# Kernel tuning notes

Measured on AMD Instinct MI355X. Metric: run time of the kernel, lower is better.

Reference implementation:

```python
import jax, jax.numpy as jnp
import numpy as np

LEAKY_SLOPE = 0.01  # torch F.leaky_relu default

N_NODES = 100000
N_EDGES = 1600000
IN_CH, HID_CH, OUT_CH = 128, 64, 32


def glorot(key, shape):
    fan_in, fan_out = shape
    lim = jnp.sqrt(6.0 / (fan_in + fan_out))
    return jax.random.uniform(key, shape, jnp.float32, -lim, lim)


def setup_inputs() -> dict:
    key = jax.random.key(0)
    ks = jax.random.split(key, 10)
    x = jax.random.normal(ks[0], (N_NODES, IN_CH), jnp.float32)
    edge_index = jax.random.randint(ks[1], (2, N_EDGES), 0, N_NODES, jnp.int64)
    return {
        "x": x,
        "edge_index": edge_index,
        "W1": glorot(ks[2], (IN_CH, HID_CH)),
        "b1": jnp.zeros((HID_CH,), jnp.float32),
        "W2": glorot(ks[3], (HID_CH, HID_CH)),
        "b2": jnp.zeros((HID_CH,), jnp.float32),
        "W_mu": glorot(ks[4], (HID_CH, OUT_CH)),
        "b_mu": jnp.zeros((OUT_CH,), jnp.float32),
        "W_ls": glorot(ks[5], (HID_CH, OUT_CH)),
        "b_ls": jnp.zeros((OUT_CH,), jnp.float32),
    }


def _gcn_norm(edge_index, n_nodes):
    """Symmetric GCN normalization with self-loops (PyG GCNConv default)."""
    src, dst = edge_index[0], edge_index[1]
    ones = jnp.ones((src.shape[0],), jnp.float32)
    deg = jax.ops.segment_sum(ones, dst, num_segments=n_nodes) + 1.0  # +1 self-loop
    dis = jax.lax.rsqrt(deg)  # deg >= 1 so no div-by-zero
    edge_w = dis[src] * dis[dst]          # [E] normalization per edge
    self_w = dis * dis                    # [N] self-loop normalization
    return src, dst, edge_w, self_w


def _gcn_conv(h, W, b, src, dst, edge_w, self_w, n_nodes):
    h = h @ W                                           # [N, C_out]
    msg = h[src] * edge_w[:, None]                      # gather + scale, [E, C_out]
    agg = jax.ops.segment_sum(msg, dst, num_segments=n_nodes)
    agg = agg + h * self_w[:, None]                     # self-loop term
    return agg + b


def reference(x, edge_index, W1, b1, W2, b2, W_mu, b_mu, W_ls, b_ls):
    n = x.shape[0]
    src, dst, ew, sw = _gcn_norm(edge_index, n)
    # dropout is identity in eval mode (reference baseline)
    h = jax.nn.leaky_relu(_gcn_conv(x, W1, b1, src, dst, ew, sw, n), LEAKY_SLOPE)
    h = jax.nn.leaky_relu(_gcn_conv(h, W2, b2, src, dst, ew, sw, n), LEAKY_SLOPE)
    mu = _gcn_conv(h, W_mu, b_mu, src, dst, ew, sw, n)
    logstd = _gcn_conv(h, W_ls, b_ls, src, dst, ew, sw, n)
    return mu, logstd
```

## Files before the change

kernel.cpp:

```cpp
#include <hip/hip_runtime.h>

#define LEAKY_SLOPE 0.01f
#define CBSH 7
#define CBSZ 128
#define CHUNK 4096

__device__ __forceinline__ unsigned short f2bf(float f) {
    unsigned int u = __builtin_bit_cast(unsigned int, f);
    u = (u + 0x7FFFu + ((u >> 16) & 1u)) >> 16;
    return (unsigned short)u;
}
__device__ __forceinline__ float bf2f(unsigned short h) {
    return __builtin_bit_cast(float, ((unsigned int)h) << 16);
}
__device__ __forceinline__ float ulof(unsigned u) {
    return __builtin_bit_cast(float, u << 16);
}
__device__ __forceinline__ float uhif(unsigned u) {
    return __builtin_bit_cast(float, u & 0xFFFF0000u);
}
__device__ __forceinline__ float bcastf(int hb, int k) {
    return __builtin_bit_cast(float, __builtin_amdgcn_readlane(hb, k));
}

__global__ __launch_bounds__(256) void chist_kernel(const int* __restrict__ dst,
                                                    int* __restrict__ cbin, int E, int ncb) {
    __shared__ int bins[1024];
    for (int i = threadIdx.x; i < 1024; i += 256) bins[i] = 0;
    __syncthreads();
    int stride = gridDim.x * blockDim.x;
    for (int e = blockIdx.x * blockDim.x + threadIdx.x; e < E; e += stride)
        atomicAdd(&bins[dst[e] >> CBSH], 1);
    __syncthreads();
    for (int i = threadIdx.x; i < ncb; i += 256) {
        int v = bins[i];
        if (v) atomicAdd(&cbin[i], v);
    }
}

__global__ __launch_bounds__(256) void cscan_kernel(const int* __restrict__ cbin,
                                                    int* __restrict__ cboff,
                                                    int* __restrict__ ccur16, int ncb) {
    __shared__ int s[256];
    __shared__ int carry;
    int t = threadIdx.x;
    if (t == 0) carry = 0;
    __syncthreads();
    for (int base = 0; base < ncb; base += 256) {
        int v = (base + t < ncb) ? cbin[base + t] : 0;
        s[t] = v;
        __syncthreads();
        for (int off = 1; off < 256; off <<= 1) {
            int u = (t >= off) ? s[t - off] : 0;
            __syncthreads();
            s[t] += u;
            __syncthreads();
        }
        int excl = carry + s[t] - v;
        if (base + t < ncb) { cboff[base + t] = excl; ccur16[(size_t)(base + t) * 16] = excl; }
        __syncthreads();
        if (t == 0) carry += s[255];
        __syncthreads();
    }
    if (t == 0) cboff[ncb] = carry;
}

__global__ __launch_bounds__(256) void scat1_kernel(const int* __restrict__ src,
                                                    const int* __restrict__ dst,
                                                    int* __restrict__ ccur16,
                                                    unsigned* __restrict__ pairs, int E) {
    __shared__ int bins[1024];
    __shared__ int base[1024];
    int t = threadIdx.x;
    for (int i = t; i < 1024; i += 256) bins[i] = 0;
    __syncthreads();
    int e0 = blockIdx.x * CHUNK;
    int m = min(CHUNK, E - e0);
    for (int i = t; i < m; i += 256)
        atomicAdd(&bins[dst[e0 + i] >> CBSH], 1);
    __syncthreads();
    for (int i = t; i < 1024; i += 256) {
        int c = bins[i];
        base[i] = c ? atomicAdd(&ccur16[(size_t)i * 16], c) : 0;
        bins[i] = 0;
    }
    __syncthreads();
    for (int i = t; i < m; i += 256) {
        int d = dst[e0 + i];
        int b = d >> CBSH;
        int off = atomicAdd(&bins[b], 1);
        pairs[base[b] + off] = (unsigned)src[e0 + i] | ((unsigned)(d & (CBSZ - 1)) << 17);
    }
}

__global__ __launch_bounds__(256) void degbuild_kernel(const unsigned* __restrict__ pairs,
                                                       const int* __restrict__ cboff,
                                                       float* __restrict__ dis,
                                                       int* __restrict__ dpad, int n) {
    __shared__ int cnt[CBSZ];
    int t = threadIdx.x;
    int b = blockIdx.x;
    if (t < CBSZ) cnt[t] = 0;
    __syncthreads();
    int e1 = cboff[b + 1];
    for (int e = cboff[b] + t; e < e1; e += 256)
        atomicAdd(&cnt[pairs[e] >> 17], 1);
    __syncthreads();
    if (t < CBSZ) {
        int node = b * CBSZ + t;
        if (node < n) {
            int d = cnt[t];
            dis[node] = rsqrtf((float)d + 1.0f);
            dpad[node] = (d + 15) & ~15;
        }
    }
}

__global__ void scan_block_sums(const int* __restrict__ deg, int* __restrict__ bsum, int n) {
    __shared__ int sdata[256];
    int i = blockIdx.x * 256 + threadIdx.x;
    int t = threadIdx.x;
    sdata[t] = (i < n) ? deg[i] : 0;
    __syncthreads();
    for (int s = 128; s > 0; s >>= 1) {
        if (t < s) sdata[t] += sdata[t + s];
        __syncthreads();
    }
    if (t == 0) bsum[blockIdx.x] = sdata[0];
}

__global__ void scan_partials(int* __restrict__ bsum, int nb, int* __restrict__ rp_end) {
    __shared__ int s[512];
    int t = threadIdx.x;
    int orig = (t < nb) ? bsum[t] : 0;
    s[t] = orig;
    __syncthreads();
    for (int off = 1; off < 512; off <<= 1) {
        int v = (t >= off) ? s[t - off] : 0;
        __syncthreads();
        s[t] += v;
        __syncthreads();
    }
    if (t < nb) bsum[t] = s[t] - orig;
    if (t == 0) rp_end[0] = s[511];
}

__global__ void scan_final(const int* __restrict__ deg, const int* __restrict__ bsum,
                           int* __restrict__ rp, int n) {
    __shared__ int s[256];
    int i = blockIdx.x * 256 + threadIdx.x;
    int t = threadIdx.x;
    int orig = (i < n) ? deg[i] : 0;
    s[t] = orig;
    __syncthreads();
    for (int off = 1; off < 256; off <<= 1) {
        int v = (t >= off) ? s[t - off] : 0;
        __syncthreads();
        s[t] += v;
        __syncthreads();
    }
    if (i < n) rp[i] = s[t] - orig + bsum[blockIdx.x];
}

__global__ __launch_bounds__(256) void scat2_kernel(const unsigned* __restrict__ pairs,
                                                    const int* __restrict__ cboff,
                                                    const int* __restrict__ rp,
                                                    int* __restrict__ ssrc, int n) {
    __shared__ int lrp[CBSZ];
    __shared__ int lcnt[CBSZ];
    int t = threadIdx.x;
    int b = blockIdx.x;
    if (t < CBSZ) {
        int node = b * CBSZ + t;
        lrp[t] = (node < n) ? rp[node] : 0;
        lcnt[t] = 0;
    }
    __syncthreads();
    int e1 = cboff[b + 1];
    for (int e = cboff[b] + t; e < e1; e += 256) {
        unsigned p = pairs[e];
        int dl = p >> 17;
        int off = atomicAdd(&lcnt[dl], 1);
        ssrc[lrp[dl] + off] = (int)(p & 0x1FFFFu);
    }
    __syncthreads();
    if (t < CBSZ) {
        int node = b * CBSZ + t;
        if (node < n) {
            int c0 = lcnt[t];
            int cpad = (c0 + 15) & ~15;
            int base = lrp[t];
            for (int i = c0; i < cpad; ++i) ssrc[base + i] = n;
        }
    }
}

__global__ __launch_bounds__(256) void gemm1_kernel(const float* __restrict__ X,
                                                    const float* __restrict__ W,
                                                    const float* __restrict__ dis,
                                                    unsigned short* __restrict__ Hh, int N) {
    __shared__ float Xs[16 * 128];
    int tid = threadIdx.x;
    int row0 = blockIdx.x * 16;
    for (int i = tid * 4; i < 16 * 128; i += 256 * 4)
        *(float4*)&Xs[i] = *(const float4*)&X[(size_t)row0 * 128 + i];
    __syncthreads();

    int c = tid & 63;
    int g = tid >> 6;
    float acc[4] = {0.f, 0.f, 0.f, 0.f};
    for (int kk = 0; kk < 128; kk += 16) {
        float w[16];
#pragma unroll
        for (int k = 0; k < 16; ++k) w[k] = W[(kk + k) * 64 + c];
#pragma unroll
        for (int r = 0; r < 4; ++r) {
            int row = g + r * 4;
#pragma unroll
            for (int k4 = 0; k4 < 16; k4 += 4) {
                float4 x4 = *(float4*)&Xs[row * 128 + kk + k4];
                acc[r] += x4.x * w[k4] + x4.y * w[k4 + 1] + x4.z * w[k4 + 2] + x4.w * w[k4 + 3];
            }
        }
    }
#pragma unroll
    for (int r = 0; r < 4; ++r) {
        int row = row0 + g + r * 4;
        Hh[(size_t)row * 64 + c] = f2bf(acc[r] * dis[row]);
    }
}

#define GATHER_WIDE(Hh, wid, lane, accv)                                       \
    float accv;                                                                \
    {                                                                          \
        int gg = (lane) >> 4, cc = (lane) & 15;                                \
        float ac0 = 0.f, ac1 = 0.f, ac2 = 0.f, ac3 = 0.f;                      \
        int e0 = rp[wid], e1 = rp[(wid) + 1];                                  \
        const int* sp = ssrc + e0;                                             \
        int cnt = e1 - e0;                                                     \
        for (int i = 0; i < cnt; i += 16) {                                    \
            int4 s4 = *(const int4*)&sp[i + gg * 4];                           \
            uint2 q0 = *(const uint2*)&Hh[(size_t)s4.x * 64 + cc * 4];         \
            uint2 q1 = *(const uint2*)&Hh[(size_t)s4.y * 64 + cc * 4];         \
            uint2 q2 = *(const uint2*)&Hh[(size_t)s4.z * 64 + cc * 4];         \
            uint2 q3 = *(const uint2*)&Hh[(size_t)s4.w * 64 + cc * 4];         \
            ac0 += (ulof(q0.x) + ulof(q1.x)) + (ulof(q2.x) + ulof(q3.x));      \
            ac1 += (uhif(q0.x) + uhif(q1.x)) + (uhif(q2.x) + uhif(q3.x));      \
            ac2 += (ulof(q0.y) + ulof(q1.y)) + (ulof(q2.y) + ulof(q3.y));      \
            ac3 += (uhif(q0.y) + uhif(q1.y)) + (uhif(q2.y) + uhif(q3.y));      \
        }                                                                      \
        ac0 += __shfl_xor(ac0, 16); ac0 += __shfl_xor(ac0, 32);                \
        ac1 += __shfl_xor(ac1, 16); ac1 += __shfl_xor(ac1, 32);                \
        ac2 += __shfl_xor(ac2, 16); ac2 += __shfl_xor(ac2, 32);                \
        ac3 += __shfl_xor(ac3, 16); ac3 += __shfl_xor(ac3, 32);                \
        int srcl = (lane) >> 2;                                                \
        float v0 = __shfl(ac0, srcl);                                          \
        float v1 = __shfl(ac1, srcl);                                          \
        float v2 = __shfl(ac2, srcl);                                          \
        float v3 = __shfl(ac3, srcl);                                          \
        int jj = (lane) & 3;                                                   \
        accv = jj == 0 ? v0 : (jj == 1 ? v1 : (jj == 2 ? v2 : v3));            \
        accv += bf2f(Hh[(size_t)(wid) * 64 + (lane)]);                         \
    }

#define LDS_MATVEC(hb, lane, Ws, o)                                            \
    float o;                                                                   \
    {                                                                          \
        float o0 = 0.f, o1 = 0.f, o2 = 0.f, o3 = 0.f;                          \
        _Pragma("unroll")                                                      \
        for (int k = 0; k < 64; k += 4) {                                      \
            o0 = fmaf(bcastf(hb, k),     Ws[(k)*64 + (lane)],     o0);         \
            o1 = fmaf(bcastf(hb, k + 1), Ws[(k+1)*64 + (lane)], o1);           \
            o2 = fmaf(bcastf(hb, k + 2), Ws[(k+2)*64 + (lane)], o2);           \
            o3 = fmaf(bcastf(hb, k + 3), Ws[(k+3)*64 + (lane)], o3);           \
        }                                                                      \
        o = (o0 + o1) + (o2 + o3);                                             \
    }

__global__ __launch_bounds__(256) void aggA_kernel(
    const unsigned short* __restrict__ Hh, const int* __restrict__ rp,
    const int* __restrict__ ssrc, const float* __restrict__ dis,
    const float* __restrict__ b1, const float* __restrict__ W2,
    unsigned short* __restrict__ Oh, int n) {
    __shared__ float Ws[64 * 64];
    for (int i = threadIdx.x * 4; i < 4096; i += 256 * 4)
        *(float4*)&Ws[i] = *(const float4*)&W2[i];
    __syncthreads();

    int lane = threadIdx.x & 63;
    float bias = b1[lane];

    int wid = (int)((blockIdx.x * blockDim.x + threadIdx.x) >> 6);
    int nwaves = (int)((gridDim.x * blockDim.x) >> 6);
    for (; wid < n; wid += nwaves) {
        GATHER_WIDE(Hh, wid, lane, accv)
        float d = dis[wid];
        float h = fmaf(accv, d, bias);
        h = h > 0.f ? h : LEAKY_SLOPE * h;
        int hb = __builtin_bit_cast(int, h);
        LDS_MATVEC(hb, lane, Ws, o)
        Oh[(size_t)wid * 64 + lane] = f2bf(o * d);
    }
}

__global__ __launch_bounds__(256) void aggB_kernel(
    const unsigned short* __restrict__ Hh, const int* __restrict__ rp,
    const int* __restrict__ ssrc, const float* __restrict__ dis,
    const float* __restrict__ b2, unsigned short* __restrict__ Oh, int n) {
    int lane = threadIdx.x & 63;
    float bias = b2[lane];
    int wid = (int)((blockIdx.x * blockDim.x + threadIdx.x) >> 6);
    int nwaves = (int)((gridDim.x * blockDim.x) >> 6);
    for (; wid < n; wid += nwaves) {
        GATHER_WIDE(Hh, wid, lane, accv)
        float d = dis[wid];
        float h = fmaf(accv, d, bias);
        h = h > 0.f ? h : LEAKY_SLOPE * h;
        Oh[(size_t)wid * 64 + lane] = f2bf(h * d);
    }
}

__global__ __launch_bounds__(256) void aggC_kernel(
    const unsigned short* __restrict__ Hh, const int* __restrict__ rp,
    const int* __restrict__ ssrc, const float* __restrict__ dis,
    const float* __restrict__ Wmu, const float* __restrict__ bmu,
    const float* __restrict__ Wls, const float* __restrict__ bls,
    float* __restrict__ mu, float* __restrict__ ls, int n) {
    __shared__ float Ws[64 * 64];
    for (int i = threadIdx.x; i < 4096; i += 256) {
        int k = i >> 6, c = i & 63;
        Ws[i] = (c < 32) ? Wmu[k * 32 + c] : Wls[k * 32 + (c - 32)];
    }
    __syncthreads();

    int lane = threadIdx.x & 63;
    int half = lane >> 5;
    int c = lane & 31;
    float bias = half ? bls[c] : bmu[c];
    float* outp = half ? ls : mu;

    int wid = (int)((blockIdx.x * blockDim.x + threadIdx.x) >> 6);
    int nwaves = (int)((gridDim.x * blockDim.x) >> 6);
    for (; wid < n; wid += nwaves) {
        GATHER_WIDE(Hh, wid, lane, accv)
        float gval = accv * dis[wid];
        int gb = __builtin_bit_cast(int, gval);
        LDS_MATVEC(gb, lane, Ws, o)
        outp[(size_t)wid * 32 + c] = o + bias;
    }
}

extern "C" void kernel_launch(void* const* d_in, const int* in_sizes, int n_in,
                              void* d_out, int out_size, void* d_ws, size_t ws_size,
                              hipStream_t stream) {
    const float* x   = (const float*)d_in[0];
    const int*   ei  = (const int*)d_in[1];
    const float* W1  = (const float*)d_in[2];
    const float* b1  = (const float*)d_in[3];
    const float* W2  = (const float*)d_in[4];
    const float* b2  = (const float*)d_in[5];
    const float* Wmu = (const float*)d_in[6];
    const float* bmu = (const float*)d_in[7];
    const float* Wls = (const float*)d_in[8];
    const float* bls = (const float*)d_in[9];

    const int N = in_sizes[0] / 128;
    const int E = in_sizes[1] / 2;
    const int NCB = (N + CBSZ - 1) / CBSZ;
    const int PADMAX = E + 15 * ((N + 15) / 16) * 16 + 64;
    const int* src  = ei;
    const int* dstp = ei + E;

    auto align64 = [](size_t v) { return (v + 63) & ~(size_t)63; };
    char* ws = (char*)d_ws;
    int*   dpad   = (int*)ws;   ws += align64((size_t)N * 4);
    float* dis    = (float*)ws; ws += align64((size_t)N * 4);
    int*   cbin   = (int*)ws;   ws += align64(1024 * 4);
    int*   cboff  = (int*)ws;   ws += align64(1025 * 4);
    int*   ccur16 = (int*)ws;   ws += align64((size_t)1024 * 16 * 4);
    int*   bsum   = (int*)ws;   ws += 4096;
    int*   rp     = (int*)ws;   ws += align64((size_t)(N + 1) * 4);
    unsigned* pairs = (unsigned*)ws; ws += align64((size_t)E * 4);
    int*   ssrc   = (int*)ws;   ws += align64((size_t)PADMAX * 4);
    unsigned short* bufH0 = (unsigned short*)ws; ws += align64(((size_t)N + 1) * 64 * 2);
    unsigned short* bufH1 = (unsigned short*)ws; ws += align64(((size_t)N + 1) * 64 * 2);

    float* mu = (float*)d_out;
    float* ls = mu + (size_t)N * 32;

    const int nblocks = (N + 255) / 256;
    const int s1blocks = (E + CHUNK - 1) / CHUNK;

    hipMemsetAsync(cbin, 0, 1024 * sizeof(int), stream);
    chist_kernel<<<256, 256, 0, stream>>>(dstp, cbin, E, NCB);
    cscan_kernel<<<1, 256, 0, stream>>>(cbin, cboff, ccur16, NCB);
    scat1_kernel<<<s1blocks, 256, 0, stream>>>(src, dstp, ccur16, pairs, E);
    degbuild_kernel<<<NCB, 256, 0, stream>>>(pairs, cboff, dis, dpad, N);
    scan_block_sums<<<nblocks, 256, 0, stream>>>(dpad, bsum, N);
    scan_partials<<<1, 512, 0, stream>>>(bsum, nblocks, rp + N);
    scan_final<<<nblocks, 256, 0, stream>>>(dpad, bsum, rp, N);
    scat2_kernel<<<NCB, 256, 0, stream>>>(pairs, cboff, rp, ssrc, N);

    gemm1_kernel<<<N / 16, 256, 0, stream>>>(x, W1, dis, bufH0, N);
    hipMemsetAsync(bufH0 + (size_t)N * 64, 0, 128, stream);
    hipMemsetAsync(bufH1 + (size_t)N * 64, 0, 128, stream);

    const int aggblocks = 2048;

    aggA_kernel<<<aggblocks, 256, 0, stream>>>(bufH0, rp, ssrc, dis, b1, W2, bufH1, N);
    aggB_kernel<<<aggblocks, 256, 0, stream>>>(bufH1, rp, ssrc, dis, b2, bufH0, N);
    aggC_kernel<<<aggblocks, 256, 0, stream>>>(bufH0, rp, ssrc, dis, Wmu, bmu,
                                               Wls, bls, mu, ls, N);
}
```

Before: 305.3 us.

## Split feature channels into slabs for cache-resident gathers and unfuse matvecs into GEMMs

Stores the bf16 hidden features as four 16-channel slabs, so each gather pass touches a 3.2 MB table that can stay in cache, and runs one gather launch per slab. The per-node LDS matvecs that were fused into the aggregation kernels move into separate tiled GEMM kernels that read fp32 intermediates from workspace, with those buffers aliased onto the dead pairs buffer and bufB. The goal is to cut random-access memory traffic in the edge gathers. The cost is 12 gather launches instead of 3, with the edge index list reread on every pass, plus extra fp32 round trips for the intermediates.

After: 484.3 us. 1.59x slower.

```diff
diff --git a/kernel.cpp b/kernel.cpp
--- a/kernel.cpp
+++ b/kernel.cpp
@@ -10,17 +10,11 @@
     u = (u + 0x7FFFu + ((u >> 16) & 1u)) >> 16;
     return (unsigned short)u;
 }
-__device__ __forceinline__ float bf2f(unsigned short h) {
-    return __builtin_bit_cast(float, ((unsigned int)h) << 16);
-}
 __device__ __forceinline__ float ulof(unsigned u) {
     return __builtin_bit_cast(float, u << 16);
 }
 __device__ __forceinline__ float uhif(unsigned u) {
     return __builtin_bit_cast(float, u & 0xFFFF0000u);
-}
-__device__ __forceinline__ float bcastf(int hb, int k) {
-    return __builtin_bit_cast(float, __builtin_amdgcn_readlane(hb, k));
 }
 
 __global__ __launch_bounds__(256) void chist_kernel(const int* __restrict__ dst,
@@ -195,10 +189,21 @@
     }
 }
 
-__global__ __launch_bounds__(256) void gemm1_kernel(const float* __restrict__ X,
-                                                    const float* __restrict__ W,
-                                                    const float* __restrict__ dis,
-                                                    unsigned short* __restrict__ Hh, int N) {
+__global__ void zerorow_kernel(unsigned* __restrict__ A, unsigned* __restrict__ B,
+                               int n, int Np1) {
+    int t = threadIdx.x;
+    int buf = t >> 5;
+    int u = t & 31;
+    int s = u >> 3, w = u & 7;
+    unsigned* p = buf ? B : A;
+    p[((size_t)s * Np1 + n) * 8 + w] = 0;
+}
+
+__global__ __launch_bounds__(256) void gemm1s_kernel(const float* __restrict__ X,
+                                                     const float* __restrict__ W,
+                                                     const float* __restrict__ dis,
+                                                     unsigned short* __restrict__ Hh,
+                                                     int N, int Np1) {
     __shared__ float Xs[16 * 128];
     int tid = threadIdx.x;
     int row0 = blockIdx.x * 16;
@@ -223,130 +228,148 @@
             }
         }
     }
+    int s = c >> 4, cc = c & 15;
 #pragma unroll
     for (int r = 0; r < 4; ++r) {
         int row = row0 + g + r * 4;
-        Hh[(size_t)row * 64 + c] = f2bf(acc[r] * dis[row]);
-    }
-}
-
-#define GATHER_WIDE(Hh, wid, lane, accv)                                       \
-    float accv;                                                                \
-    {                                                                          \
-        int gg = (lane) >> 4, cc = (lane) & 15;                                \
-        float ac0 = 0.f, ac1 = 0.f, ac2 = 0.f, ac3 = 0.f;                      \
-        int e0 = rp[wid], e1 = rp[(wid) + 1];                                  \
-        const int* sp = ssrc + e0;                                             \
-        int cnt = e1 - e0;                                                     \
-        for (int i = 0; i < cnt; i += 16) {                                    \
-            int4 s4 = *(const int4*)&sp[i + gg * 4];                           \
-            uint2 q0 = *(const uint2*)&Hh[(size_t)s4.x * 64 + cc * 4];         \
-            uint2 q1 = *(const uint2*)&Hh[(size_t)s4.y * 64 + cc * 4];         \
-            uint2 q2 = *(const uint2*)&Hh[(size_t)s4.z * 64 + cc * 4];         \
-            uint2 q3 = *(const uint2*)&Hh[(size_t)s4.w * 64 + cc * 4];         \
-            ac0 += (ulof(q0.x) + ulof(q1.x)) + (ulof(q2.x) + ulof(q3.x));      \
-            ac1 += (uhif(q0.x) + uhif(q1.x)) + (uhif(q2.x) + uhif(q3.x));      \
-            ac2 += (ulof(q0.y) + ulof(q1.y)) + (ulof(q2.y) + ulof(q3.y));      \
-            ac3 += (uhif(q0.y) + uhif(q1.y)) + (uhif(q2.y) + uhif(q3.y));      \
-        }                                                                      \
-        ac0 += __shfl_xor(ac0, 16); ac0 += __shfl_xor(ac0, 32);                \
-        ac1 += __shfl_xor(ac1, 16); ac1 += __shfl_xor(ac1, 32);                \
-        ac2 += __shfl_xor(ac2, 16); ac2 += __shfl_xor(ac2, 32);                \
-        ac3 += __shfl_xor(ac3, 16); ac3 += __shfl_xor(ac3, 32);                \
-        int srcl = (lane) >> 2;                                                \
-        float v0 = __shfl(ac0, srcl);                                          \
-        float v1 = __shfl(ac1, srcl);                                          \
-        float v2 = __shfl(ac2, srcl);                                          \
-        float v3 = __shfl(ac3, srcl);                                          \
-        int jj = (lane) & 3;                                                   \
-        accv = jj == 0 ? v0 : (jj == 1 ? v1 : (jj == 2 ? v2 : v3));            \
-        accv += bf2f(Hh[(size_t)(wid) * 64 + (lane)]);                         \
-    }
-
-#define LDS_MATVEC(hb, lane, Ws, o)                                            \
-    float o;                                                                   \
-    {                                                                          \
-        float o0 = 0.f, o1 = 0.f, o2 = 0.f, o3 = 0.f;                          \
-        _Pragma("unroll")                                                      \
-        for (int k = 0; k < 64; k += 4) {                                      \
-            o0 = fmaf(bcastf(hb, k),     Ws[(k)*64 + (lane)],     o0);         \
-            o1 = fmaf(bcastf(hb, k + 1), Ws[(k+1)*64 + (lane)], o1);           \
-            o2 = fmaf(bcastf(hb, k + 2), Ws[(k+2)*64 + (lane)], o2);           \
-            o3 = fmaf(bcastf(hb, k + 3), Ws[(k+3)*64 + (lane)], o3);           \
-        }                                                                      \
-        o = (o0 + o1) + (o2 + o3);                                             \
-    }
-
-__global__ __launch_bounds__(256) void aggA_kernel(
-    const unsigned short* __restrict__ Hh, const int* __restrict__ rp,
+        Hh[((size_t)s * Np1 + row) * 16 + cc] = f2bf(acc[r] * dis[row]);
+    }
+}
+
+template <int MODE>
+__global__ __launch_bounds__(256) void sgather_kernel(
+    const unsigned* __restrict__ Hsrc, const int* __restrict__ rp,
     const int* __restrict__ ssrc, const float* __restrict__ dis,
-    const float* __restrict__ b1, const float* __restrict__ W2,
-    unsigned short* __restrict__ Oh, int n) {
-    __shared__ float Ws[64 * 64];
-    for (int i = threadIdx.x * 4; i < 4096; i += 256 * 4)
-        *(float4*)&Ws[i] = *(const float4*)&W2[i];
-    __syncthreads();
-
+    const float* __restrict__ bias, void* __restrict__ outp,
+    int n, int Np1, int s) {
     int lane = threadIdx.x & 63;
-    float bias = b1[lane];
+    int g = lane >> 3, p = lane & 7;
+    const unsigned* Hs = Hsrc + (size_t)s * Np1 * 8;
+
+    float2 bv = make_float2(0.f, 0.f);
+    if (MODE < 2) bv = *(const float2*)&bias[s * 16 + 2 * p];
 
     int wid = (int)((blockIdx.x * blockDim.x + threadIdx.x) >> 6);
     int nwaves = (int)((gridDim.x * blockDim.x) >> 6);
     for (; wid < n; wid += nwaves) {
-        GATHER_WIDE(Hh, wid, lane, accv)
+        int e0 = rp[wid];
+        int e1 = rp[wid + 1];
+        const int* sp = ssrc + e0;
+        int cnt = e1 - e0;
+        float a0 = 0.f, a1 = 0.f;
+        for (int i = 0; i < cnt; i += 16) {
+            int2 s2 = *(const int2*)&sp[i + 2 * g];
+            unsigned q0 = Hs[(size_t)s2.x * 8 + p];
+            unsigned q1 = Hs[(size_t)s2.y * 8 + p];
+            a0 += ulof(q0) + ulof(q1);
+            a1 += uhif(q0) + uhif(q1);
+        }
+        a0 += __shfl_xor(a0, 8); a0 += __shfl_xor(a0, 16); a0 += __shfl_xor(a0, 32);
+        a1 += __shfl_xor(a1, 8); a1 += __shfl_xor(a1, 16); a1 += __shfl_xor(a1, 32);
+        unsigned qs = Hs[(size_t)wid * 8 + p];
+        a0 += ulof(qs);
+        a1 += uhif(qs);
         float d = dis[wid];
-        float h = fmaf(accv, d, bias);
-        h = h > 0.f ? h : LEAKY_SLOPE * h;
-        int hb = __builtin_bit_cast(int, h);
-        LDS_MATVEC(hb, lane, Ws, o)
-        Oh[(size_t)wid * 64 + lane] = f2bf(o * d);
-    }
-}
-
-__global__ __launch_bounds__(256) void aggB_kernel(
-    const unsigned short* __restrict__ Hh, const int* __restrict__ rp,
-    const int* __restrict__ ssrc, const float* __restrict__ dis,
-    const float* __restrict__ b2, unsigned short* __restrict__ Oh, int n) {
-    int lane = threadIdx.x & 63;
-    float bias = b2[lane];
-    int wid = (int)((blockIdx.x * blockDim.x + threadIdx.x) >> 6);
-    int nwaves = (int)((gridDim.x * blockDim.x) >> 6);
-    for (; wid < n; wid += nwaves) {
-        GATHER_WIDE(Hh, wid, lane, accv)
-        float d = dis[wid];
-        float h = fmaf(accv, d, bias);
-        h = h > 0.f ? h : LEAKY_SLOPE * h;
-        Oh[(size_t)wid * 64 + lane] = f2bf(h * d);
-    }
-}
-
-__global__ __launch_bounds__(256) void aggC_kernel(
-    const unsigned short* __restrict__ Hh, const int* __restrict__ rp,
-    const int* __restrict__ ssrc, const float* __restrict__ dis,
-    const float* __restrict__ Wmu, const float* __restrict__ bmu,
-    const float* __restrict__ Wls, const float* __restrict__ bls,
-    float* __restrict__ mu, float* __restrict__ ls, int n) {
-    __shared__ float Ws[64 * 64];
-    for (int i = threadIdx.x; i < 4096; i += 256) {
-        int k = i >> 6, c = i & 63;
-        Ws[i] = (c < 32) ? Wmu[k * 32 + c] : Wls[k * 32 + (c - 32)];
-    }
-    __syncthreads();
-
-    int lane = threadIdx.x & 63;
-    int half = lane >> 5;
-    int c = lane & 31;
-    float bias = half ? bls[c] : bmu[c];
+        if (MODE == 0) {
+            float h0 = fmaf(a0, d, bv.x);
+            float h1 = fmaf(a1, d, bv.y);
+            h0 = h0 > 0.f ? h0 : LEAKY_SLOPE * h0;
+            h1 = h1 > 0.f ? h1 : LEAKY_SLOPE * h1;
+            if (g == 0)
+                *(float2*)&((float*)outp)[(size_t)wid * 64 + s * 16 + 2 * p] = make_float2(h0, h1);
+        } else if (MODE == 1) {
+            float h0 = fmaf(a0, d, bv.x);
+            float h1 = fmaf(a1, d, bv.y);
+            h0 = (h0 > 0.f ? h0 : LEAKY_SLOPE * h0) * d;
+            h1 = (h1 > 0.f ? h1 : LEAKY_SLOPE * h1) * d;
+            unsigned u = (unsigned)f2bf(h0) | ((unsigned)f2bf(h1) << 16);
+            if (g == 0)
+                ((unsigned*)outp)[((size_t)s * Np1 + wid) * 8 + p] = u;
+        } else {
+            float g0 = a0 * d;
+            float g1 = a1 * d;
+            if (g == 0)
+                *(float2*)&((float*)outp)[(size_t)wid * 64 + s * 16 + 2 * p] = make_float2(g0, g1);
+        }
+    }
+}
+
+__global__ __launch_bounds__(256) void gemmA_kernel(const float* __restrict__ h1,
+                                                    const float* __restrict__ W2,
+                                                    const float* __restrict__ dis,
+                                                    unsigned short* __restrict__ Hh,
+                                                    int N, int Np1) {
+    __shared__ float Xs[16 * 64];
+    int tid = threadIdx.x;
+    int row0 = blockIdx.x * 16;
+    *(float4*)&Xs[tid * 4] = *(const float4*)&h1[(size_t)row0 * 64 + tid * 4];
+    __syncthreads();
+
+    int c = tid & 63;
+    int g = tid >> 6;
+    float acc[4] = {0.f, 0.f, 0.f, 0.f};
+    for (int kk = 0; kk < 64; kk += 16) {
+        float w[16];
+#pragma unroll
+        for (int k = 0; k < 16; ++k) w[k] = W2[(kk + k) * 64 + c];
+#pragma unroll
+        for (int r = 0; r < 4; ++r) {
+            int row = g + r * 4;
+#pragma unroll
+            for (int k4 = 0; k4 < 16; k4 += 4) {
+                float4 x4 = *(float4*)&Xs[row * 64 + kk + k4];
+                acc[r] += x4.x * w[k4] + x4.y * w[k4 + 1] + x4.z * w[k4 + 2] + x4.w * w[k4 + 3];
+            }
+        }
+    }
+    int s = c >> 4, cc = c & 15;
+#pragma unroll
+    for (int r = 0; r < 4; ++r) {
+        int row = row0 + g + r * 4;
+        Hh[((size_t)s * Np1 + row) * 16 + cc] = f2bf(acc[r] * dis[row]);
+    }
+}
+
+__global__ __launch_bounds__(256) void gemmC_kernel(const float* __restrict__ gbuf,
+                                                    const float* __restrict__ Wmu,
+                                                    const float* __restrict__ bmu,
+                                                    const float* __restrict__ Wls,
+                                                    const float* __restrict__ bls,
+                                                    float* __restrict__ mu,
+                                                    float* __restrict__ ls, int N) {
+    __shared__ float Xs[16 * 64];
+    int tid = threadIdx.x;
+    int row0 = blockIdx.x * 16;
+    *(float4*)&Xs[tid * 4] = *(const float4*)&gbuf[(size_t)row0 * 64 + tid * 4];
+    __syncthreads();
+
+    int c = tid & 63;
+    int g = tid >> 6;
+    int half = c >> 5;
+    int cc = c & 31;
+    const float* Wp = half ? Wls : Wmu;
+    float bias = half ? bls[cc] : bmu[cc];
     float* outp = half ? ls : mu;
 
-    int wid = (int)((blockIdx.x * blockDim.x + threadIdx.x) >> 6);
-    int nwaves = (int)((gridDim.x * blockDim.x) >> 6);
-    for (; wid < n; wid += nwaves) {
-        GATHER_WIDE(Hh, wid, lane, accv)
-        float gval = accv * dis[wid];
-        int gb = __builtin_bit_cast(int, gval);
-        LDS_MATVEC(gb, lane, Ws, o)
-        outp[(size_t)wid * 32 + c] = o + bias;
+    float acc[4] = {0.f, 0.f, 0.f, 0.f};
+    for (int kk = 0; kk < 64; kk += 16) {
+        float w[16];
+#pragma unroll
+        for (int k = 0; k < 16; ++k) w[k] = Wp[(kk + k) * 32 + cc];
+#pragma unroll
+        for (int r = 0; r < 4; ++r) {
+            int row = g + r * 4;
+#pragma unroll
+            for (int k4 = 0; k4 < 16; k4 += 4) {
+                float4 x4 = *(float4*)&Xs[row * 64 + kk + k4];
+                acc[r] += x4.x * w[k4] + x4.y * w[k4 + 1] + x4.z * w[k4 + 2] + x4.w * w[k4 + 3];
+            }
+        }
+    }
+#pragma unroll
+    for (int r = 0; r < 4; ++r) {
+        int row = row0 + g + r * 4;
+        outp[(size_t)row * 32 + cc] = acc[r] + bias;
     }
 }
 
@@ -366,6 +389,7 @@
 
     const int N = in_sizes[0] / 128;
     const int E = in_sizes[1] / 2;
+    const int Np1 = N + 1;
     const int NCB = (N + CBSZ - 1) / CBSZ;
     const int PADMAX = E + 15 * ((N + 15) / 16) * 16 + 64;
     const int* src  = ei;
@@ -380,16 +404,20 @@
     int*   ccur16 = (int*)ws;   ws += align64((size_t)1024 * 16 * 4);
     int*   bsum   = (int*)ws;   ws += 4096;
     int*   rp     = (int*)ws;   ws += align64((size_t)(N + 1) * 4);
-    unsigned* pairs = (unsigned*)ws; ws += align64((size_t)E * 4);
     int*   ssrc   = (int*)ws;   ws += align64((size_t)PADMAX * 4);
-    unsigned short* bufH0 = (unsigned short*)ws; ws += align64(((size_t)N + 1) * 64 * 2);
-    unsigned short* bufH1 = (unsigned short*)ws; ws += align64(((size_t)N + 1) * 64 * 2);
+    unsigned short* bufA = (unsigned short*)ws; ws += align64((size_t)Np1 * 128);
+    unsigned short* bufB = (unsigned short*)ws; ws += align64((size_t)Np1 * 128);
+    unsigned* pairs = (unsigned*)ws;            ws += align64((size_t)E * 4);
+    ws += align64((size_t)N * 64 * 4 - (size_t)E * 4 + 64);
+    float* h1buf = (float*)pairs;
+    float* gbuf  = (float*)bufB;
 
     float* mu = (float*)d_out;
     float* ls = mu + (size_t)N * 32;
 
     const int nblocks = (N + 255) / 256;
     const int s1blocks = (E + CHUNK - 1) / CHUNK;
+    const int aggblocks = 2048;
 
     hipMemsetAsync(cbin, 0, 1024 * sizeof(int), stream);
     chist_kernel<<<256, 256, 0, stream>>>(dstp, cbin, E, NCB);
@@ -401,14 +429,22 @@
     scan_final<<<nblocks, 256, 0, stream>>>(dpad, bsum, rp, N);
     scat2_kernel<<<NCB, 256, 0, stream>>>(pairs, cboff, rp, ssrc, N);
 
-    gemm1_kernel<<<N / 16, 256, 0, stream>>>(x, W1, dis, bufH0, N);
-    hipMemsetAsync(bufH0 + (size_t)N * 64, 0, 128, stream);
-    hipMemsetAsync(bufH1 + (size_t)N * 64, 0, 128, stream);
-
-    const int aggblocks = 2048;
-
-    aggA_kernel<<<aggblocks, 256, 0, stream>>>(bufH0, rp, ssrc, dis, b1, W2, bufH1, N);
-    aggB_kernel<<<aggblocks, 256, 0, stream>>>(bufH1, rp, ssrc, dis, b2, bufH0, N);
-    aggC_kernel<<<aggblocks, 256, 0, stream>>>(bufH0, rp, ssrc, dis, Wmu, bmu,
-                                               Wls, bls, mu, ls, N);
-}
+    zerorow_kernel<<<1, 64, 0, stream>>>((unsigned*)bufA, (unsigned*)bufB, N, Np1);
+
+    gemm1s_kernel<<<N / 16, 256, 0, stream>>>(x, W1, dis, bufA, N, Np1);
+    for (int s = 0; s < 4; ++s)
+        sgather_kernel<0><<<aggblocks, 256, 0, stream>>>((const unsigned*)bufA, rp, ssrc,
+                                                         dis, b1, h1buf, N, Np1, s);
+
+    gemmA_kernel<<<N / 16, 256, 0, stream>>>(h1buf, W2, dis, bufB, N, Np1);
+
+    for (int s = 0; s < 4; ++s)
+        sgather_kernel<1><<<aggblocks, 256, 0, stream>>>((const unsigned*)bufB, rp, ssrc,
+                                                         dis, b2, bufA, N, Np1, s);
+
+    for (int s = 0; s < 4; ++s)
+        sgather_kernel<2><<<aggblocks, 256, 0, stream>>>((const unsigned*)bufA, rp, ssrc,
+                                                         dis, nullptr, gbuf, N, Np1, s);
+
+    gemmC_kernel<<<N / 16, 256, 0, stream>>>(gbuf, Wmu, bmu, Wls, bls, mu, ls, N);
+}
```

## Fuse degree, scan and scatter into one per-bucket CSR build kernel with slack

Applied to the files above, without the earlier changes.

Replaces the degree kernel, three-pass global prefix scan and second scatter kernel with one bucket kernel. Each 128-node bucket counts degrees, does a local shared-memory scan of padded counts and writes sources into a slack-padded region starting at e0 + b*SLACK. Aggregation kernels now read a per-node start and padded count instead of a global row pointer. This removes four kernel launches and their global passes, at the cost of a larger ssrc buffer. Correctness relies on each bucket's padding fitting within SLACK (at most 15*128 = 1920). The histogram grid is also raised to 1024 blocks.

Result: slower. 337.4 us (+10.5%).

```diff
diff --git a/kernel.cpp b/kernel.cpp
--- a/kernel.cpp
+++ b/kernel.cpp
@@ -4,6 +4,7 @@
 #define CBSH 7
 #define CBSZ 128
 #define CHUNK 4096
+#define SLACK 2048
 
 __device__ __forceinline__ unsigned short f2bf(float f) {
     unsigned int u = __builtin_bit_cast(unsigned int, f);
@@ -93,104 +94,59 @@
     }
 }
 
-__global__ __launch_bounds__(256) void degbuild_kernel(const unsigned* __restrict__ pairs,
-                                                       const int* __restrict__ cboff,
-                                                       float* __restrict__ dis,
-                                                       int* __restrict__ dpad, int n) {
+__global__ __launch_bounds__(256) void bucket_kernel(const unsigned* __restrict__ pairs,
+                                                     const int* __restrict__ cboff,
+                                                     float* __restrict__ dis,
+                                                     int* __restrict__ rpS,
+                                                     int* __restrict__ rcnt,
+                                                     int* __restrict__ ssrc, int n) {
     __shared__ int cnt[CBSZ];
+    __shared__ int incl[CBSZ];
+    __shared__ int lcur[CBSZ];
     int t = threadIdx.x;
     int b = blockIdx.x;
     if (t < CBSZ) cnt[t] = 0;
     __syncthreads();
-    int e1 = cboff[b + 1];
-    for (int e = cboff[b] + t; e < e1; e += 256)
+    int e0 = cboff[b], e1 = cboff[b + 1];
+    for (int e = e0 + t; e < e1; e += 256)
         atomicAdd(&cnt[pairs[e] >> 17], 1);
+    __syncthreads();
+    if (t < CBSZ) incl[t] = (cnt[t] + 15) & ~15;
+    __syncthreads();
+    for (int off = 1; off < CBSZ; off <<= 1) {
+        int v = 0;
+        if (t < CBSZ && t >= off) v = incl[t - off];
+        __syncthreads();
+        if (t < CBSZ) incl[t] += v;
+        __syncthreads();
+    }
+    int base = e0 + b * SLACK;
+    if (t < CBSZ) {
+        int pc = (cnt[t] + 15) & ~15;
+        int excl = incl[t] - pc;
+        lcur[t] = excl;
+        int node = b * CBSZ + t;
+        if (node < n) {
+            rpS[node]  = base + excl;
+            rcnt[node] = pc;
+            dis[node]  = rsqrtf((float)cnt[t] + 1.0f);
+        }
+    }
+    __syncthreads();
+    for (int e = e0 + t; e < e1; e += 256) {
+        unsigned p = pairs[e];
+        int dl = p >> 17;
+        int off = atomicAdd(&lcur[dl], 1);
+        ssrc[base + off] = (int)(p & 0x1FFFFu);
+    }
     __syncthreads();
     if (t < CBSZ) {
         int node = b * CBSZ + t;
         if (node < n) {
-            int d = cnt[t];
-            dis[node] = rsqrtf((float)d + 1.0f);
-            dpad[node] = (d + 15) & ~15;
-        }
-    }
-}
-
-__global__ void scan_block_sums(const int* __restrict__ deg, int* __restrict__ bsum, int n) {
-    __shared__ int sdata[256];
-    int i = blockIdx.x * 256 + threadIdx.x;
-    int t = threadIdx.x;
-    sdata[t] = (i < n) ? deg[i] : 0;
-    __syncthreads();
-    for (int s = 128; s > 0; s >>= 1) {
-        if (t < s) sdata[t] += sdata[t + s];
-        __syncthreads();
-    }
-    if (t == 0) bsum[blockIdx.x] = sdata[0];
-}
-
-__global__ void scan_partials(int* __restrict__ bsum, int nb, int* __restrict__ rp_end) {
-    __shared__ int s[512];
-    int t = threadIdx.x;
-    int orig = (t < nb) ? bsum[t] : 0;
-    s[t] = orig;
-    __syncthreads();
-    for (int off = 1; off < 512; off <<= 1) {
-        int v = (t >= off) ? s[t - off] : 0;
-        __syncthreads();
-        s[t] += v;
-        __syncthreads();
-    }
-    if (t < nb) bsum[t] = s[t] - orig;
-    if (t == 0) rp_end[0] = s[511];
-}
-
-__global__ void scan_final(const int* __restrict__ deg, const int* __restrict__ bsum,
-                           int* __restrict__ rp, int n) {
-    __shared__ int s[256];
-    int i = blockIdx.x * 256 + threadIdx.x;
-    int t = threadIdx.x;
-    int orig = (i < n) ? deg[i] : 0;
-    s[t] = orig;
-    __syncthreads();
-    for (int off = 1; off < 256; off <<= 1) {
-        int v = (t >= off) ? s[t - off] : 0;
-        __syncthreads();
-        s[t] += v;
-        __syncthreads();
-    }
-    if (i < n) rp[i] = s[t] - orig + bsum[blockIdx.x];
-}
-
-__global__ __launch_bounds__(256) void scat2_kernel(const unsigned* __restrict__ pairs,
-                                                    const int* __restrict__ cboff,
-                                                    const int* __restrict__ rp,
-                                                    int* __restrict__ ssrc, int n) {
-    __shared__ int lrp[CBSZ];
-    __shared__ int lcnt[CBSZ];
-    int t = threadIdx.x;
-    int b = blockIdx.x;
-    if (t < CBSZ) {
-        int node = b * CBSZ + t;
-        lrp[t] = (node < n) ? rp[node] : 0;
-        lcnt[t] = 0;
-    }
-    __syncthreads();
-    int e1 = cboff[b + 1];
-    for (int e = cboff[b] + t; e < e1; e += 256) {
-        unsigned p = pairs[e];
-        int dl = p >> 17;
-        int off = atomicAdd(&lcnt[dl], 1);
-        ssrc[lrp[dl] + off] = (int)(p & 0x1FFFFu);
-    }
-    __syncthreads();
-    if (t < CBSZ) {
-        int node = b * CBSZ + t;
-        if (node < n) {
-            int c0 = lcnt[t];
-            int cpad = (c0 + 15) & ~15;
-            int base = lrp[t];
-            for (int i = c0; i < cpad; ++i) ssrc[base + i] = n;
+            int c0 = cnt[t];
+            int pc = (c0 + 15) & ~15;
+            int excl = incl[t] - pc;
+            for (int i = excl + c0; i < excl + pc; ++i) ssrc[base + i] = n;
         }
     }
 }
@@ -235,9 +191,8 @@
     {                                                                          \
         int gg = (lane) >> 4, cc = (lane) & 15;                                \
         float ac0 = 0.f, ac1 = 0.f, ac2 = 0.f, ac3 = 0.f;                      \
-        int e0 = rp[wid], e1 = rp[(wid) + 1];                                  \
-        const int* sp = ssrc + e0;                                             \
-        int cnt = e1 - e0;                                                     \
+        const int* sp = ssrc + rpS[wid];                                       \
+        int cnt = rcnt[wid];                                                   \
         for (int i = 0; i < cnt; i += 16) {                                    \
             int4 s4 = *(const int4*)&sp[i + gg * 4];                           \
             uint2 q0 = *(const uint2*)&Hh[(size_t)s4.x * 64 + cc * 4];         \
@@ -278,10 +233,10 @@
     }
 
 __global__ __launch_bounds__(256) void aggA_kernel(
-    const unsigned short* __restrict__ Hh, const int* __restrict__ rp,
-    const int* __restrict__ ssrc, const float* __restrict__ dis,
-    const float* __restrict__ b1, const float* __restrict__ W2,
-    unsigned short* __restrict__ Oh, int n) {
+    const unsigned short* __restrict__ Hh, const int* __restrict__ rpS,
+    const int* __restrict__ rcnt, const int* __restrict__ ssrc,
+    const float* __restrict__ dis, const float* __restrict__ b1,
+    const float* __restrict__ W2, unsigned short* __restrict__ Oh, int n) {
     __shared__ float Ws[64 * 64];
     for (int i = threadIdx.x * 4; i < 4096; i += 256 * 4)
         *(float4*)&Ws[i] = *(const float4*)&W2[i];
@@ -304,9 +259,10 @@
 }
 
 __global__ __launch_bounds__(256) void aggB_kernel(
-    const unsigned short* __restrict__ Hh, const int* __restrict__ rp,
-    const int* __restrict__ ssrc, const float* __restrict__ dis,
-    const float* __restrict__ b2, unsigned short* __restrict__ Oh, int n) {
+    const unsigned short* __restrict__ Hh, const int* __restrict__ rpS,
+    const int* __restrict__ rcnt, const int* __restrict__ ssrc,
+    const float* __restrict__ dis, const float* __restrict__ b2,
+    unsigned short* __restrict__ Oh, int n) {
     int lane = threadIdx.x & 63;
     float bias = b2[lane];
     int wid = (int)((blockIdx.x * blockDim.x + threadIdx.x) >> 6);
@@ -321,11 +277,12 @@
 }
 
 __global__ __launch_bounds__(256) void aggC_kernel(
-    const unsigned short* __restrict__ Hh, const int* __restrict__ rp,
-    const int* __restrict__ ssrc, const float* __restrict__ dis,
-    const float* __restrict__ Wmu, const float* __restrict__ bmu,
-    const float* __restrict__ Wls, const float* __restrict__ bls,
-    float* __restrict__ mu, float* __restrict__ ls, int n) {
+    const unsigned short* __restrict__ Hh, const int* __restrict__ rpS,
+    const int* __restrict__ rcnt, const int* __restrict__ ssrc,
+    const float* __restrict__ dis, const float* __restrict__ Wmu,
+    const float* __restrict__ bmu, const float* __restrict__ Wls,
+    const float* __restrict__ bls, float* __restrict__ mu,
+    float* __restrict__ ls, int n) {
     __shared__ float Ws[64 * 64];
     for (int i = threadIdx.x; i < 4096; i += 256) {
         int k = i >> 6, c = i & 63;
@@ -367,39 +324,33 @@
     const int N = in_sizes[0] / 128;
     const int E = in_sizes[1] / 2;
     const int NCB = (N + CBSZ - 1) / CBSZ;
-    const int PADMAX = E + 15 * ((N + 15) / 16) * 16 + 64;
+    const int SSRC_SZ = E + NCB * SLACK + 64;
     const int* src  = ei;
     const int* dstp = ei + E;
 
     auto align64 = [](size_t v) { return (v + 63) & ~(size_t)63; };
     char* ws = (char*)d_ws;
-    int*   dpad   = (int*)ws;   ws += align64((size_t)N * 4);
     float* dis    = (float*)ws; ws += align64((size_t)N * 4);
     int*   cbin   = (int*)ws;   ws += align64(1024 * 4);
     int*   cboff  = (int*)ws;   ws += align64(1025 * 4);
     int*   ccur16 = (int*)ws;   ws += align64((size_t)1024 * 16 * 4);
-    int*   bsum   = (int*)ws;   ws += 4096;
-    int*   rp     = (int*)ws;   ws += align64((size_t)(N + 1) * 4);
+    int*   rpS    = (int*)ws;   ws += align64((size_t)N * 4);
+    int*   rcnt   = (int*)ws;   ws += align64((size_t)N * 4);
     unsigned* pairs = (unsigned*)ws; ws += align64((size_t)E * 4);
-    int*   ssrc   = (int*)ws;   ws += align64((size_t)PADMAX * 4);
+    int*   ssrc   = (int*)ws;   ws += align64((size_t)SSRC_SZ * 4);
     unsigned short* bufH0 = (unsigned short*)ws; ws += align64(((size_t)N + 1) * 64 * 2);
     unsigned short* bufH1 = (unsigned short*)ws; ws += align64(((size_t)N + 1) * 64 * 2);
 
     float* mu = (float*)d_out;
     float* ls = mu + (size_t)N * 32;
 
-    const int nblocks = (N + 255) / 256;
     const int s1blocks = (E + CHUNK - 1) / CHUNK;
 
     hipMemsetAsync(cbin, 0, 1024 * sizeof(int), stream);
-    chist_kernel<<<256, 256, 0, stream>>>(dstp, cbin, E, NCB);
+    chist_kernel<<<1024, 256, 0, stream>>>(dstp, cbin, E, NCB);
     cscan_kernel<<<1, 256, 0, stream>>>(cbin, cboff, ccur16, NCB);
     scat1_kernel<<<s1blocks, 256, 0, stream>>>(src, dstp, ccur16, pairs, E);
-    degbuild_kernel<<<NCB, 256, 0, stream>>>(pairs, cboff, dis, dpad, N);
-    scan_block_sums<<<nblocks, 256, 0, stream>>>(dpad, bsum, N);
-    scan_partials<<<1, 512, 0, stream>>>(bsum, nblocks, rp + N);
-    scan_final<<<nblocks, 256, 0, stream>>>(dpad, bsum, rp, N);
-    scat2_kernel<<<NCB, 256, 0, stream>>>(pairs, cboff, rp, ssrc, N);
+    bucket_kernel<<<NCB, 256, 0, stream>>>(pairs, cboff, dis, rpS, rcnt, ssrc, N);
 
     gemm1_kernel<<<N / 16, 256, 0, stream>>>(x, W1, dis, bufH0, N);
     hipMemsetAsync(bufH0 + (size_t)N * 64, 0, 128, stream);
@@ -407,8 +358,8 @@
 
     const int aggblocks = 2048;
 
-    aggA_kernel<<<aggblocks, 256, 0, stream>>>(bufH0, rp, ssrc, dis, b1, W2, bufH1, N);
-    aggB_kernel<<<aggblocks, 256, 0, stream>>>(bufH1, rp, ssrc, dis, b2, bufH0, N);
-    aggC_kernel<<<aggblocks, 256, 0, stream>>>(bufH0, rp, ssrc, dis, Wmu, bmu,
+    aggA_kernel<<<aggblocks, 256, 0, stream>>>(bufH0, rpS, rcnt, ssrc, dis, b1, W2, bufH1, N);
+    aggB_kernel<<<aggblocks, 256, 0, stream>>>(bufH1, rpS, rcnt, ssrc, dis, b2, bufH0, N);
+    aggC_kernel<<<aggblocks, 256, 0, stream>>>(bufH0, rpS, rcnt, ssrc, dis, Wmu, bmu,
                                                Wls, bls, mu, ls, N);
 }
```
